# Optimization experiments

Hardware: AMD Instinct MI355X
Metric: run time of the kernel (lower is better)

## Reference

```python
import math
import jax, jax.numpy as jnp
import numpy as np
from jax import lax

B, M, L, DM = 4, 4, 1024, 768
DS, DCONV, LR = 8, 3, 16
D2 = DM // 2                # d_inner // 2 (expand=1)
DTR = math.ceil(DM / 16)    # dt_rank = 48
LN_EPS = 1e-5
RMS_EPS = 1e-5


def setup_inputs() -> dict:
    key = jax.random.key(0)
    ks = jax.random.split(key, 10)
    hidden_states = jax.random.normal(ks[0], (B, M, L, DM), jnp.float32)
    modality_index = jnp.arange(M, dtype=jnp.int32)
    in_w1 = jax.random.normal(ks[1], (M, LR, DM), jnp.float32) / np.sqrt(DM)
    in_ln_g = jnp.ones((M, LR), jnp.float32)
    in_ln_b = jnp.zeros((M, LR), jnp.float32)
    in_w2 = jax.random.normal(ks[2], (M, DM, LR), jnp.float32) / np.sqrt(LR)
    x_proj_w = jax.random.normal(ks[3], (DTR + 2 * DS, D2), jnp.float32) / np.sqrt(D2)
    dt_proj_w = jax.random.uniform(ks[4], (D2, DTR), jnp.float32, -DTR ** -0.5, DTR ** -0.5)
    dt = jnp.exp(jax.random.uniform(ks[5], (D2,), jnp.float32) * (np.log(0.1) - np.log(0.001)) + np.log(0.001))
    dt = jnp.clip(dt, 1e-4, None)
    dt_proj_b = dt + jnp.log(-jnp.expm1(-dt))   # inverse-softplus init
    A_log = jnp.log(jnp.broadcast_to(jnp.arange(1, DS + 1, dtype=jnp.float32), (D2, DS)))
    D = jnp.ones((D2,), jnp.float32)
    conv_x_w = jax.random.uniform(ks[6], (D2, 1, DCONV), jnp.float32, -DCONV ** -0.5, DCONV ** -0.5)
    conv_z_w = jax.random.uniform(ks[7], (D2, 1, DCONV), jnp.float32, -DCONV ** -0.5, DCONV ** -0.5)
    norm_w = jnp.ones((D2,), jnp.float32)
    out_w = jax.random.normal(ks[8], (M, DM, D2), jnp.float32) / np.sqrt(D2)
    scale = jnp.float32(1e-4)
    return dict(hidden_states=hidden_states, in_w1=in_w1, in_ln_g=in_ln_g, in_ln_b=in_ln_b,
                in_w2=in_w2, x_proj_w=x_proj_w, dt_proj_w=dt_proj_w, dt_proj_b=dt_proj_b,
                A_log=A_log, D=D, conv_x_w=conv_x_w, conv_z_w=conv_z_w, norm_w=norm_w,
                out_w=out_w, scale=scale, modality_index=modality_index)


def _dwconv_silu(x, w):
    # x: (b, d, L), w: (d, 1, k); depthwise 'same' conv (no bias: conv_bias//2 == 0) + SiLU
    y = lax.conv_general_dilated(x, w, (1,), 'SAME', feature_group_count=x.shape[1],
                                 dimension_numbers=('NCH', 'OIH', 'NCH'))
    return jax.nn.silu(y)


def _combine(e1, e2):
    a1, b1 = e1
    a2, b2 = e2
    return a1 * a2, a2 * b1 + b2


def reference(hidden_states, in_w1, in_ln_g, in_ln_b, in_w2, x_proj_w, dt_proj_w, dt_proj_b,
              A_log, D, conv_x_w, conv_z_w, norm_w, out_w, scale, modality_index):
    b, m, l, dm = hidden_states.shape
    d2 = conv_x_w.shape[0]
    dtr, ds = dt_proj_w.shape[1], A_log.shape[1]
    # --- per-modality low-rank in-projection: Linear -> LayerNorm -> GELU -> Linear ---
    w1 = jnp.take(in_w1, modality_index, axis=0)
    g = jnp.take(in_ln_g, modality_index, axis=0)[None, :, None, :]
    bta = jnp.take(in_ln_b, modality_index, axis=0)[None, :, None, :]
    w2 = jnp.take(in_w2, modality_index, axis=0)
    t = jnp.einsum('bmld,mrd->bmlr', hidden_states, w1)
    mu = t.mean(-1, keepdims=True)
    var = jnp.mean((t - mu) ** 2, -1, keepdims=True)
    t = (t - mu) * lax.rsqrt(var + LN_EPS) * g + bta
    t = jax.nn.gelu(t, approximate=False)
    xz = jnp.einsum('bmlr,mdr->bmld', t, w2)          # (b, m, l, d_inner)
    xz = xz.transpose(0, 2, 1, 3).reshape(b, l * m, -1)  # modality-interleaved, (b, Lm, d_inner)
    x, z = jnp.split(xz, 2, axis=-1)
    # --- depthwise conv + SiLU on both branches ---
    x = _dwconv_silu(x.transpose(0, 2, 1), conv_x_w)  # (b, d2, Lm)
    z = _dwconv_silu(z.transpose(0, 2, 1), conv_z_w)
    xT = x.transpose(0, 2, 1)  # (b, Lm, d2)
    zT = z.transpose(0, 2, 1)
    # --- input-dependent SSM parameters ---
    x_dbl = xT @ x_proj_w.T                              # (b, Lm, dtr+2*ds)
    dt, Bc, Cc = jnp.split(x_dbl, [dtr, dtr + ds], axis=-1)
    dt = dt @ dt_proj_w.T + dt_proj_b                    # Linear WITH bias (as in source)
    delta = jax.nn.softplus(dt + dt_proj_b)             # delta_bias added again (faithful)
    A = -jnp.exp(A_log)                                  # (d2, ds)
    dA = jnp.exp(delta[..., None] * A)                   # (b, Lm, d2, ds)
    dBx = delta[..., None] * Bc[:, :, None, :] * xT[..., None]
    # --- selective scan: h_t = dA_t * h_{t-1} + dBx_t ---
    _, h = lax.associative_scan(_combine, (dA, dBx), axis=1)
    y = jnp.einsum('blds,bls->bld', h, Cc) + D * xT      # (b, Lm, d2)
    # --- gated RMSNorm (norm before gate) ---
    y = y * lax.rsqrt(jnp.mean(y * y, -1, keepdims=True) + RMS_EPS) * norm_w
    y = y * jax.nn.silu(zT)
    # --- per-modality out-projection ---
    y = y.reshape(b, l, m, d2).transpose(0, 2, 1, 3)     # (b, m, l, d2)
    out = jnp.einsum('bmld,mod->bmlo', y, jnp.take(out_w, modality_index, axis=0))
    return out * scale
```

## Files before the change

### kernel.cpp

```cpp
#include <hip/hip_runtime.h>
#include <hip/hip_bf16.h>

#define LM   4096
#define D2   384
#define NCHK 64
#define TCHK 64

typedef __attribute__((ext_vector_type(8))) short short8b;
typedef __attribute__((ext_vector_type(4))) float f32x4;

__device__ __forceinline__ float siluf_(float x) { return x / (1.f + expf(-x)); }
__device__ __forceinline__ float softplusf_(float x) {
  return fmaxf(x, 0.f) + log1pf(expf(-fabsf(x)));
}
__device__ __forceinline__ short f2b_(float f) {
  __hip_bfloat16 h = __float2bfloat16(f);
  return *reinterpret_cast<short*>(&h);
}

__global__ __launch_bounds__(256) void k1a_proj(
    const float* __restrict__ hs, const float* __restrict__ w1g,
    const float* __restrict__ lng, const float* __restrict__ lnb,
    const int* __restrict__ midx, float* __restrict__ tbuf)
{
  __shared__ float w1s[16][772];
  const int tid = threadIdx.x;
  const int l0 = blockIdx.x * 16;
  const int m  = blockIdx.y;
  const int b  = blockIdx.z;
  const int mi = midx[m];
  {
    const float4* wp = (const float4*)(w1g + (size_t)mi * 16 * 768);
    for (int i = tid; i < 16 * 192; i += 256) {
      int r = i / 192, c = (i % 192) * 4;
      *(float4*)&w1s[r][c] = wp[i];
    }
  }
  __syncthreads();
  const int p = tid >> 4, r = tid & 15;
  const float* hrow = hs + (((size_t)(b * 4 + m)) * 1024 + l0 + p) * 768;
  float a0 = 0.f, a1 = 0.f, a2 = 0.f, a3 = 0.f;
  #pragma unroll 4
  for (int k = 0; k < 192; k += 4) {
    float4 x0 = *(const float4*)&hrow[(k + 0) * 4];
    float4 x1 = *(const float4*)&hrow[(k + 1) * 4];
    float4 x2 = *(const float4*)&hrow[(k + 2) * 4];
    float4 x3 = *(const float4*)&hrow[(k + 3) * 4];
    float4 w0 = *(const float4*)&w1s[r][(k + 0) * 4];
    float4 w1 = *(const float4*)&w1s[r][(k + 1) * 4];
    float4 w2 = *(const float4*)&w1s[r][(k + 2) * 4];
    float4 w3 = *(const float4*)&w1s[r][(k + 3) * 4];
    a0 += x0.x*w0.x + x0.y*w0.y + x0.z*w0.z + x0.w*w0.w;
    a1 += x1.x*w1.x + x1.y*w1.y + x1.z*w1.z + x1.w*w1.w;
    a2 += x2.x*w2.x + x2.y*w2.y + x2.z*w2.z + x2.w*w2.w;
    a3 += x3.x*w3.x + x3.y*w3.y + x3.z*w3.z + x3.w*w3.w;
  }
  const float acc = (a0 + a1) + (a2 + a3);
  float s = acc, q = acc * acc;
  #pragma unroll
  for (int msk = 1; msk < 16; msk <<= 1) {
    s += __shfl_xor(s, msk);
    q += __shfl_xor(q, msk);
  }
  const float mu  = s * (1.f / 16.f);
  const float var = q * (1.f / 16.f) - mu * mu;
  float v = (acc - mu) * rsqrtf(var + 1e-5f) * lng[mi * 16 + r] + lnb[mi * 16 + r];
  v = 0.5f * v * (1.f + erff(v * 0.70710678118654752f));
  tbuf[(((size_t)(b * 4 + m)) * 1024 + l0 + p) * 16 + r] = v;
}

__global__ __launch_bounds__(256) void k1b_xz(
    const float* __restrict__ tbuf, const float* __restrict__ w2g,
    const int* __restrict__ midx,
    float* __restrict__ xr, float* __restrict__ zr)
{
  __shared__ float ts[32][16];
  const int tid = threadIdx.x;
  const int l0 = blockIdx.x * 32;
  const int m  = blockIdx.y;
  const int b  = blockIdx.z;
  const int mi = midx[m];
  if (tid < 128) {
    float4 v = *(const float4*)&tbuf[(((size_t)(b * 4 + m)) * 1024 + l0) * 16 + tid * 4];
    *(float4*)&ts[tid >> 2][(tid & 3) * 4] = v;
  }
  float w2c[3][16];
  #pragma unroll
  for (int dd = 0; dd < 3; dd++) {
    const int d = tid + 256 * dd;
    #pragma unroll
    for (int rq = 0; rq < 4; rq++)
      *(float4*)&w2c[dd][rq * 4] = *(const float4*)&w2g[((size_t)mi * 768 + d) * 16 + rq * 4];
  }
  __syncthreads();
  for (int p = 0; p < 32; p++) {
    float tv[16];
    #pragma unroll
    for (int rq = 0; rq < 4; rq++) *(float4*)&tv[rq * 4] = *(const float4*)&ts[p][rq * 4];
    const int t = (l0 + p) * 4 + m;
    const size_t o = ((size_t)b * LM + t) * D2;
    #pragma unroll
    for (int dd = 0; dd < 3; dd++) {
      float a = 0.f;
      #pragma unroll
      for (int r2 = 0; r2 < 16; r2++) a += tv[r2] * w2c[dd][r2];
      const int d = tid + 256 * dd;
      if (d < D2) xr[o + d] = a;
      else        zr[o + d - D2] = a;
    }
  }
}

__global__ __launch_bounds__(256) void k2_xdbl(
    const float* __restrict__ xr, const float* __restrict__ xw,
    const float* __restrict__ cwx, float* __restrict__ xdbl)
{
  __shared__ float xcl[16][388];
  __shared__ float xws[32][388];
  const int tid = threadIdx.x;
  const int t0 = blockIdx.x * 16;
  const int b  = blockIdx.y;

  for (int i = tid; i < 16 * 384; i += 256) {
    const int tt = i / 384, d = i % 384;
    const int t = t0 + tt;
    const size_t base = (size_t)b * LM * D2 + d;
    float xm = (t > 0)      ? xr[base + (size_t)(t - 1) * D2] : 0.f;
    float x0 =                xr[base + (size_t)t * D2];
    float xp = (t + 1 < LM) ? xr[base + (size_t)(t + 1) * D2] : 0.f;
    float v = cwx[d * 3] * xm + cwx[d * 3 + 1] * x0 + cwx[d * 3 + 2] * xp;
    xcl[tt][d] = siluf_(v);
  }

  #pragma unroll
  for (int pass = 0; pass < 2; pass++) {
    if (pass) __syncthreads();
    {
      const float4* wp = (const float4*)(xw + (size_t)pass * 32 * 384);
      for (int i = tid; i < 32 * 96; i += 256) {
        int o = i / 96, c = (i % 96) * 4;
        *(float4*)&xws[o][c] = wp[i];
      }
    }
    __syncthreads();
    const int ks  = tid & 3;
    const int mt  = tid >> 2;
    const int og4 = mt & 7;
    const int ttg = mt >> 3;
    float acc[2][4] = {};
    for (int q = ks * 24; q < ks * 24 + 24; q++) {
      float4 a[2], w[4];
      #pragma unroll
      for (int i = 0; i < 2; i++) a[i] = *(const float4*)&xcl[ttg * 2 + i][q * 4];
      #pragma unroll
      for (int j = 0; j < 4; j++) w[j] = *(const float4*)&xws[og4 * 4 + j][q * 4];
      #pragma unroll
      for (int i = 0; i < 2; i++)
        #pragma unroll
        for (int j = 0; j < 4; j++)
          acc[i][j] += a[i].x * w[j].x + a[i].y * w[j].y + a[i].z * w[j].z + a[i].w * w[j].w;
    }
    #pragma unroll
    for (int i = 0; i < 2; i++)
      #pragma unroll
      for (int j = 0; j < 4; j++) {
        float v = acc[i][j];
        v += __shfl_xor(v, 1);  v += __shfl_xor(v, 2);
        acc[i][j] = v;
      }
    if (ks == 0) {
      #pragma unroll
      for (int i = 0; i < 2; i++) {
        float4 v4 = make_float4(acc[i][0], acc[i][1], acc[i][2], acc[i][3]);
        *(float4*)&xdbl[((size_t)b * LM + t0 + ttg * 2 + i) * 64 + pass * 32 + og4 * 4] = v4;
      }
    }
  }
}

__global__ __launch_bounds__(384) void k3_delta(
    const float* __restrict__ xdbl, const float* __restrict__ dtw,
    const float* __restrict__ dtb, float* __restrict__ delta)
{
  __shared__ float xt[32][48];
  const int tid = threadIdx.x;
  const int t0 = blockIdx.x * 32;
  const int b  = blockIdx.y;
  for (int i = tid; i < 32 * 12; i += 384) {
    int tt = i / 12, c = (i % 12) * 4;
    *(float4*)&xt[tt][c] = *(const float4*)&xdbl[((size_t)b * LM + t0 + tt) * 64 + c];
  }
  float wc[48];
  #pragma unroll
  for (int rq = 0; rq < 12; rq++)
    *(float4*)&wc[rq * 4] = *(const float4*)&dtw[(size_t)tid * 48 + rq * 4];
  const float bias2 = 2.f * dtb[tid];
  __syncthreads();
  for (int p = 0; p < 32; p++) {
    float acc = 0.f;
    #pragma unroll
    for (int r2 = 0; r2 < 48; r2++) acc += xt[p][r2] * wc[r2];
    delta[((size_t)b * LM + t0 + p) * D2 + tid] = softplusf_(acc + bias2);
  }
}

__global__ __launch_bounds__(768) void s1_scan(
    const float* __restrict__ xr, const float* __restrict__ delta,
    const float* __restrict__ xdbl, const float* __restrict__ alog,
    const float* __restrict__ cwx, float* __restrict__ aP, float* __restrict__ bAg)
{
  __shared__ float Bs[TCHK][8];
  const int tid = threadIdx.x;
  const int half = tid >= 384 ? 1 : 0;
  const int d = tid - half * 384;
  const int c = blockIdx.x, b = blockIdx.y;
  const int t0 = c * TCHK;
  for (int i = tid; i < TCHK * 8; i += 768) {
    const int tt = i >> 3, s = i & 7;
    Bs[tt][s] = xdbl[((size_t)b * LM + t0 + tt) * 64 + 48 + s];
  }
  float a[4];
  #pragma unroll
  for (int s = 0; s < 4; s++) a[s] = -expf(alog[d * 8 + half * 4 + s]);
  const float w0 = cwx[d * 3], w1 = cwx[d * 3 + 1], w2 = cwx[d * 3 + 2];
  const float* xp = xr + (size_t)b * LM * D2 + d;
  const float* dp = delta + (size_t)b * LM * D2 + d;
  float xm = (t0 > 0) ? xp[(size_t)(t0 - 1) * D2] : 0.f;
  float x0 = xp[(size_t)t0 * D2];
  float h[4] = {};
  float ap[4] = {1.f, 1.f, 1.f, 1.f};
  __syncthreads();
  for (int tt = 0; tt < TCHK; tt++) {
    const int t = t0 + tt;
    const float xn = (t + 1 < LM) ? xp[(size_t)(t + 1) * D2] : 0.f;
    const float xc = siluf_(w0 * xm + w1 * x0 + w2 * xn);
    const float dv = dp[(size_t)t * D2];
    #pragma unroll
    for (int s = 0; s < 4; s++) {
      const float dA = expf(dv * a[s]);
      ap[s] *= dA;
      h[s] = dA * h[s] + (dv * Bs[tt][half * 4 + s]) * xc;
    }
    xm = x0; x0 = xn;
  }
  const size_t o = (((size_t)b * NCHK + c) * 8 + half * 4) * D2 + d;
  #pragma unroll
  for (int s = 0; s < 4; s++) { aP[o + (size_t)s * D2] = ap[s]; bAg[o + (size_t)s * D2] = h[s]; }
}

__global__ __launch_bounds__(256) void s2_combine(
    const float* __restrict__ aP, const float* __restrict__ bAg, float* __restrict__ hI)
{
  const int idx = blockIdx.x * 256 + threadIdx.x;
  const int d = idx % 384;
  const int s = (idx / 384) & 7;
  const int b = idx / 3072;
  float h = 0.f;
  for (int c = 0; c < NCHK; c++) {
    const size_t o = (((size_t)b * NCHK + c) * 8 + s) * D2 + d;
    const float av = aP[o], bv = bAg[o];
    hI[o] = h;
    h = av * h + bv;
  }
}

__global__ __launch_bounds__(256) void wconv(
    const float* __restrict__ w, short* __restrict__ w16)
{
  const int i = (blockIdx.x * 256 + threadIdx.x) * 4;
  const float4 v = *(const float4*)&w[i];
  ushort4 o;
  o.x = (unsigned short)f2b_(v.x);
  o.y = (unsigned short)f2b_(v.y);
  o.z = (unsigned short)f2b_(v.z);
  o.w = (unsigned short)f2b_(v.w);
  *(ushort4*)&w16[i] = o;
}

__global__ __launch_bounds__(384) void s3_rescan(
    const float* __restrict__ xr, const float* __restrict__ zr,
    const float* delta_in, const float* __restrict__ xdbl,
    const float* __restrict__ hI, const float* __restrict__ alog,
    const float* __restrict__ cwx, const float* __restrict__ cwz,
    const float* __restrict__ Dv, const float* __restrict__ nw,
    float* Yg)
{
  __shared__ float Bs[TCHK][8];
  __shared__ float Cs[TCHK][8];
  __shared__ float yt[32][389];
  __shared__ float part[32][12];
  __shared__ float rinv[32];
  const int tid = threadIdx.x;
  const int d = tid;
  const int c = blockIdx.x, b = blockIdx.y;
  const int t0 = c * TCHK;
  for (int i = tid; i < TCHK * 8; i += 384) {
    const int tt = i >> 3, s = i & 7;
    const size_t o = ((size_t)b * LM + t0 + tt) * 64;
    Bs[tt][s] = xdbl[o + 48 + s];
    Cs[tt][s] = xdbl[o + 56 + s];
  }
  float a[8];
  #pragma unroll
  for (int s = 0; s < 8; s++) a[s] = -expf(alog[d * 8 + s]);
  float h[8];
  const size_t ho = (((size_t)b * NCHK + c) * 8) * D2 + d;
  #pragma unroll
  for (int s = 0; s < 8; s++) h[s] = hI[ho + (size_t)s * D2];
  const float wx0 = cwx[d * 3], wx1 = cwx[d * 3 + 1], wx2 = cwx[d * 3 + 2];
  const float wz0 = cwz[d * 3], wz1 = cwz[d * 3 + 1], wz2 = cwz[d * 3 + 2];
  const float Dd = Dv[d], nwd = nw[d];
  const float* xp = xr + (size_t)b * LM * D2 + d;
  const float* zp = zr + (size_t)b * LM * D2 + d;
  const float* dp = delta_in + (size_t)b * LM * D2 + d;
  float xm = (t0 > 0) ? xp[(size_t)(t0 - 1) * D2] : 0.f;
  float x0 = xp[(size_t)t0 * D2];
  float zm = (t0 > 0) ? zp[(size_t)(t0 - 1) * D2] : 0.f;
  float z0 = zp[(size_t)t0 * D2];
  __syncthreads();

  #pragma unroll
  for (int H = 0; H < 2; H++) {
    const int tb = t0 + H * 32;
    for (int tt = 0; tt < 32; tt++) {
      const int t = tb + tt;
      const float xn = (t + 1 < LM) ? xp[(size_t)(t + 1) * D2] : 0.f;
      const float xc = siluf_(wx0 * xm + wx1 * x0 + wx2 * xn);
      const float dv = dp[(size_t)t * D2];
      float yv = 0.f;
      #pragma unroll
      for (int s = 0; s < 8; s++) {
        const float dA = expf(dv * a[s]);
        h[s] = dA * h[s] + (dv * Bs[H * 32 + tt][s]) * xc;
        yv += h[s] * Cs[H * 32 + tt][s];
      }
      yv += Dd * xc;
      yt[tt][d] = yv;
      xm = x0; x0 = xn;
    }
    __syncthreads();
    {
      const int tr = tid & 31, j = tid >> 5;
      float sum = 0.f;
      #pragma unroll
      for (int k = 0; k < 32; k++) { const float v = yt[tr][j * 32 + k]; sum += v * v; }
      part[tr][j] = sum;
    }
    __syncthreads();
    if (tid < 32) {
      float sm = 0.f;
      #pragma unroll
      for (int j = 0; j < 12; j++) sm += part[tid][j];
      rinv[tid] = rsqrtf(sm * (1.f / 384.f) + 1e-5f);
    }
    __syncthreads();
    for (int tt = 0; tt < 32; tt++) {
      const int t = tb + tt;
      const float zn = (t + 1 < LM) ? zp[(size_t)(t + 1) * D2] : 0.f;
      const float zc = siluf_(siluf_(wz0 * zm + wz1 * z0 + wz2 * zn));
      Yg[((size_t)b * LM + t) * D2 + d] = yt[tt][d] * rinv[tt] * nwd * zc;
      zm = z0; z0 = zn;
    }
    __syncthreads();
  }
}

__global__ __launch_bounds__(256) void k4_mfma(
    const float* __restrict__ Yg, const short* __restrict__ W16,
    const int* __restrict__ midx, const float* __restrict__ scalep,
    float* __restrict__ out)
{
  const int tid = threadIdx.x;
  const int wid = tid >> 6, lane = tid & 63;
  const int lt = blockIdx.x, ot = blockIdx.y, bm = blockIdx.z;
  const int b = bm >> 2, m = bm & 3;
  const int mi = midx[m];
  const int l0 = lt * 128, o0 = ot * 128;
  const int wr = wid >> 1, wc = wid & 1;
  const int lr = lane & 15, lg = lane >> 4;
  const float scale = scalep[0];

  const float* Ab = Yg + (size_t)b * LM * D2;
  const short* Bb = W16 + (size_t)mi * 768 * D2;

  f32x4 acc[4][4];
  #pragma unroll
  for (int i = 0; i < 4; i++)
    #pragma unroll
    for (int j = 0; j < 4; j++) acc[i][j] = (f32x4){0.f, 0.f, 0.f, 0.f};

  for (int k0 = 0; k0 < D2; k0 += 32) {
    const int kk = k0 + lg * 8;
    short8b afr[4], bfr[4];
    #pragma unroll
    for (int mr = 0; mr < 4; mr++) {
      const int row = l0 + wr * 64 + mr * 16 + lr;
      const float* ap = Ab + (size_t)(row * 4 + m) * D2 + kk;
      const f32x4 a0 = *(const f32x4*)ap;
      const f32x4 a1 = *(const f32x4*)(ap + 4);
      short8b af;
      af[0] = f2b_(a0.x); af[1] = f2b_(a0.y); af[2] = f2b_(a0.z); af[3] = f2b_(a0.w);
      af[4] = f2b_(a1.x); af[5] = f2b_(a1.y); af[6] = f2b_(a1.z); af[7] = f2b_(a1.w);
      afr[mr] = af;
    }
    #pragma unroll
    for (int nr = 0; nr < 4; nr++) {
      const int col = o0 + wc * 64 + nr * 16 + lr;
      bfr[nr] = *(const short8b*)(Bb + (size_t)col * D2 + kk);
    }
    #pragma unroll
    for (int mr = 0; mr < 4; mr++)
      #pragma unroll
      for (int nr = 0; nr < 4; nr++)
        acc[mr][nr] = __builtin_amdgcn_mfma_f32_16x16x32_bf16(
            afr[mr], bfr[nr], acc[mr][nr], 0, 0, 0);
  }

  #pragma unroll
  for (int mr = 0; mr < 4; mr++) {
    #pragma unroll
    for (int r = 0; r < 4; r++) {
      const int row = l0 + wr * 64 + mr * 16 + lg * 4 + r;
      const size_t ob = (((size_t)(b * 4 + m)) * 1024 + row) * 768;
      #pragma unroll
      for (int nr = 0; nr < 4; nr++) {
        const int col = o0 + wc * 64 + nr * 16 + lr;
        out[ob + col] = acc[mr][nr][r] * scale;
      }
    }
  }
}

extern "C" void kernel_launch(void* const* d_in, const int* in_sizes, int n_in,
                              void* d_out, int out_size, void* d_ws, size_t ws_size,
                              hipStream_t stream)
{
  const float* hs   = (const float*)d_in[0];
  const float* w1   = (const float*)d_in[1];
  const float* lng  = (const float*)d_in[2];
  const float* lnb  = (const float*)d_in[3];
  const float* w2   = (const float*)d_in[4];
  const float* xw   = (const float*)d_in[5];
  const float* dtw  = (const float*)d_in[6];
  const float* dtb  = (const float*)d_in[7];
  const float* alog = (const float*)d_in[8];
  const float* Dv   = (const float*)d_in[9];
  const float* cwx  = (const float*)d_in[10];
  const float* cwz  = (const float*)d_in[11];
  const float* nw   = (const float*)d_in[12];
  const float* ow   = (const float*)d_in[13];
  const float* sc   = (const float*)d_in[14];
  const int*   midx = (const int*)d_in[15];
  float* out = (float*)d_out;

  float* ws = (float*)d_ws;
  const size_t NE = (size_t)4 * LM * D2;
  float* xr    = ws;
  float* zr    = xr + NE;
  float* delta = zr + NE;
  float* xdbl  = delta + NE;
  float* aP    = xdbl + (size_t)4 * LM * 64;
  float* bAg   = aP + (size_t)4 * NCHK * 8 * D2;
  float* hI    = bAg + (size_t)4 * NCHK * 8 * D2;
  float* tbuf  = aP;
  short* owb16 = (short*)aP;

  k1a_proj<<<dim3(64, 4, 4), 256, 0, stream>>>(hs, w1, lng, lnb, midx, tbuf);
  k1b_xz<<<dim3(32, 4, 4), 256, 0, stream>>>(tbuf, w2, midx, xr, zr);
  k2_xdbl<<<dim3(256, 4), 256, 0, stream>>>(xr, xw, cwx, xdbl);
  k3_delta<<<dim3(128, 4), 384, 0, stream>>>(xdbl, dtw, dtb, delta);
  s1_scan<<<dim3(NCHK, 4), 768, 0, stream>>>(xr, delta, xdbl, alog, cwx, aP, bAg);
  s2_combine<<<48, 256, 0, stream>>>(aP, bAg, hI);
  wconv<<<1152, 256, 0, stream>>>(ow, owb16);
  s3_rescan<<<dim3(NCHK, 4), 384, 0, stream>>>(xr, zr, delta, xdbl, hI, alog, cwx, cwz, Dv, nw, delta);
  k4_mfma<<<dim3(8, 6, 16), 256, 0, stream>>>(delta, owb16, midx, sc, out);
}
```

Before: 462.6 us.

## Halve scan chunk size, derive dA by powers of one exp, reuse output buffer

Scan chunks drop from 64 to 32 timesteps, doubling the blocks in s1_scan and s3_rescan, so the serial per-thread chain is shorter and more work is in flight. When A rows are geometric (A_s = (s+1)·A_1, detected at runtime), the per-state exps are replaced by one exp plus repeated multiplications, with a fallback to per-state exp otherwise. The chunk carries now live in the output buffer and s2 writes the prefix in place, freeing workspace. In exchange the s2 serial combine chain doubles in length, and the power products may differ slightly in rounding from separate exps.

```diff
diff --git a/kernel.cpp b/kernel.cpp
--- a/kernel.cpp
+++ b/kernel.cpp
@@ -1,10 +1,10 @@
 #include <hip/hip_runtime.h>
 #include <hip/hip_bf16.h>
 
-#define LM   4096
-#define D2   384
-#define NCHK 64
-#define TCHK 64
+#define LM    4096
+#define D2    384
+#define NCHK2 128
+#define TC2   32
 
 typedef __attribute__((ext_vector_type(8))) short short8b;
 typedef __attribute__((ext_vector_type(4))) float f32x4;
@@ -209,19 +209,25 @@
     const float* __restrict__ xdbl, const float* __restrict__ alog,
     const float* __restrict__ cwx, float* __restrict__ aP, float* __restrict__ bAg)
 {
-  __shared__ float Bs[TCHK][8];
+  __shared__ float Bs[TC2][8];
   const int tid = threadIdx.x;
   const int half = tid >= 384 ? 1 : 0;
   const int d = tid - half * 384;
   const int c = blockIdx.x, b = blockIdx.y;
-  const int t0 = c * TCHK;
-  for (int i = tid; i < TCHK * 8; i += 768) {
-    const int tt = i >> 3, s = i & 7;
+  const int t0 = c * TC2;
+  if (tid < TC2 * 8) {
+    const int tt = tid >> 3, s = tid & 7;
     Bs[tt][s] = xdbl[((size_t)b * LM + t0 + tt) * 64 + 48 + s];
   }
+  const float a1 = -expf(alog[d * 8]);
   float a[4];
-  #pragma unroll
-  for (int s = 0; s < 4; s++) a[s] = -expf(alog[d * 8 + half * 4 + s]);
+  bool geo = true;
+  #pragma unroll
+  for (int s = 0; s < 4; s++) {
+    a[s] = -expf(alog[d * 8 + half * 4 + s]);
+    const float ex = (float)(half * 4 + s + 1) * a1;
+    geo = geo && (fabsf(a[s] - ex) <= 1e-4f * fabsf(a[s]));
+  }
   const float w0 = cwx[d * 3], w1 = cwx[d * 3 + 1], w2 = cwx[d * 3 + 2];
   const float* xp = xr + (size_t)b * LM * D2 + d;
   const float* dp = delta + (size_t)b * LM * D2 + d;
@@ -230,36 +236,48 @@
   float h[4] = {};
   float ap[4] = {1.f, 1.f, 1.f, 1.f};
   __syncthreads();
-  for (int tt = 0; tt < TCHK; tt++) {
+  #pragma unroll 4
+  for (int tt = 0; tt < TC2; tt++) {
     const int t = t0 + tt;
     const float xn = (t + 1 < LM) ? xp[(size_t)(t + 1) * D2] : 0.f;
     const float xc = siluf_(w0 * xm + w1 * x0 + w2 * xn);
     const float dv = dp[(size_t)t * D2];
+    float dA[4];
+    if (geo) {
+      const float q = expf(dv * a1);
+      const float q2 = q * q, q4 = q2 * q2;
+      if (half == 0) { dA[0] = q;      dA[1] = q2;      dA[2] = q2 * q;      dA[3] = q4; }
+      else           { dA[0] = q4 * q; dA[1] = q4 * q2; dA[2] = q4 * q2 * q; dA[3] = q4 * q4; }
+    } else {
+      #pragma unroll
+      for (int s = 0; s < 4; s++) dA[s] = expf(dv * a[s]);
+    }
+    const float dx = dv * xc;
     #pragma unroll
     for (int s = 0; s < 4; s++) {
-      const float dA = expf(dv * a[s]);
-      ap[s] *= dA;
-      h[s] = dA * h[s] + (dv * Bs[tt][half * 4 + s]) * xc;
+      ap[s] *= dA[s];
+      h[s] = dA[s] * h[s] + dx * Bs[tt][half * 4 + s];
     }
     xm = x0; x0 = xn;
   }
-  const size_t o = (((size_t)b * NCHK + c) * 8 + half * 4) * D2 + d;
+  const size_t o = (((size_t)b * NCHK2 + c) * 8 + half * 4) * D2 + d;
   #pragma unroll
   for (int s = 0; s < 4; s++) { aP[o + (size_t)s * D2] = ap[s]; bAg[o + (size_t)s * D2] = h[s]; }
 }
 
 __global__ __launch_bounds__(256) void s2_combine(
-    const float* __restrict__ aP, const float* __restrict__ bAg, float* __restrict__ hI)
+    float* __restrict__ aP, const float* __restrict__ bAg)
 {
   const int idx = blockIdx.x * 256 + threadIdx.x;
   const int d = idx % 384;
   const int s = (idx / 384) & 7;
   const int b = idx / 3072;
   float h = 0.f;
-  for (int c = 0; c < NCHK; c++) {
-    const size_t o = (((size_t)b * NCHK + c) * 8 + s) * D2 + d;
+  #pragma unroll 4
+  for (int c = 0; c < NCHK2; c++) {
+    const size_t o = (((size_t)b * NCHK2 + c) * 8 + s) * D2 + d;
     const float av = aP[o], bv = bAg[o];
-    hI[o] = h;
+    aP[o] = h;
     h = av * h + bv;
   }
 }
@@ -285,26 +303,32 @@
     const float* __restrict__ Dv, const float* __restrict__ nw,
     float* Yg)
 {
-  __shared__ float Bs[TCHK][8];
-  __shared__ float Cs[TCHK][8];
-  __shared__ float yt[32][389];
-  __shared__ float part[32][12];
-  __shared__ float rinv[32];
+  __shared__ float Bs[TC2][8];
+  __shared__ float Cs[TC2][8];
+  __shared__ float yt[TC2][389];
+  __shared__ float part[TC2][12];
+  __shared__ float rinv[TC2];
   const int tid = threadIdx.x;
   const int d = tid;
   const int c = blockIdx.x, b = blockIdx.y;
-  const int t0 = c * TCHK;
-  for (int i = tid; i < TCHK * 8; i += 384) {
-    const int tt = i >> 3, s = i & 7;
+  const int t0 = c * TC2;
+  if (tid < TC2 * 8) {
+    const int tt = tid >> 3, s = tid & 7;
     const size_t o = ((size_t)b * LM + t0 + tt) * 64;
     Bs[tt][s] = xdbl[o + 48 + s];
     Cs[tt][s] = xdbl[o + 56 + s];
   }
+  const float a1 = -expf(alog[d * 8]);
   float a[8];
-  #pragma unroll
-  for (int s = 0; s < 8; s++) a[s] = -expf(alog[d * 8 + s]);
+  bool geo = true;
+  #pragma unroll
+  for (int s = 0; s < 8; s++) {
+    a[s] = -expf(alog[d * 8 + s]);
+    const float ex = (float)(s + 1) * a1;
+    geo = geo && (fabsf(a[s] - ex) <= 1e-4f * fabsf(a[s]));
+  }
   float h[8];
-  const size_t ho = (((size_t)b * NCHK + c) * 8) * D2 + d;
+  const size_t ho = (((size_t)b * NCHK2 + c) * 8) * D2 + d;
   #pragma unroll
   for (int s = 0; s < 8; s++) h[s] = hI[ho + (size_t)s * D2];
   const float wx0 = cwx[d * 3], wx1 = cwx[d * 3 + 1], wx2 = cwx[d * 3 + 2];
@@ -315,53 +339,60 @@
   const float* dp = delta_in + (size_t)b * LM * D2 + d;
   float xm = (t0 > 0) ? xp[(size_t)(t0 - 1) * D2] : 0.f;
   float x0 = xp[(size_t)t0 * D2];
+  __syncthreads();
+
+  #pragma unroll 4
+  for (int tt = 0; tt < TC2; tt++) {
+    const int t = t0 + tt;
+    const float xn = (t + 1 < LM) ? xp[(size_t)(t + 1) * D2] : 0.f;
+    const float xc = siluf_(wx0 * xm + wx1 * x0 + wx2 * xn);
+    const float dv = dp[(size_t)t * D2];
+    float dA[8];
+    if (geo) {
+      const float q = expf(dv * a1);
+      const float q2 = q * q, q4 = q2 * q2;
+      dA[0] = q;      dA[1] = q2;      dA[2] = q2 * q;      dA[3] = q4;
+      dA[4] = q4 * q; dA[5] = q4 * q2; dA[6] = q4 * q2 * q; dA[7] = q4 * q4;
+    } else {
+      #pragma unroll
+      for (int s = 0; s < 8; s++) dA[s] = expf(dv * a[s]);
+    }
+    const float dx = dv * xc;
+    float yv = 0.f;
+    #pragma unroll
+    for (int s = 0; s < 8; s++) {
+      h[s] = dA[s] * h[s] + dx * Bs[tt][s];
+      yv += h[s] * Cs[tt][s];
+    }
+    yv += Dd * xc;
+    yt[tt][d] = yv;
+    xm = x0; x0 = xn;
+  }
+  __syncthreads();
+  {
+    const int tr = tid & 31, j = tid >> 5;
+    float sum = 0.f;
+    #pragma unroll
+    for (int k = 0; k < 32; k++) { const float v = yt[tr][j * 32 + k]; sum += v * v; }
+    part[tr][j] = sum;
+  }
+  __syncthreads();
+  if (tid < TC2) {
+    float sm = 0.f;
+    #pragma unroll
+    for (int j = 0; j < 12; j++) sm += part[tid][j];
+    rinv[tid] = rsqrtf(sm * (1.f / 384.f) + 1e-5f);
+  }
+  __syncthreads();
   float zm = (t0 > 0) ? zp[(size_t)(t0 - 1) * D2] : 0.f;
   float z0 = zp[(size_t)t0 * D2];
-  __syncthreads();
-
-  #pragma unroll
-  for (int H = 0; H < 2; H++) {
-    const int tb = t0 + H * 32;
-    for (int tt = 0; tt < 32; tt++) {
-      const int t = tb + tt;
-      const float xn = (t + 1 < LM) ? xp[(size_t)(t + 1) * D2] : 0.f;
-      const float xc = siluf_(wx0 * xm + wx1 * x0 + wx2 * xn);
-      const float dv = dp[(size_t)t * D2];
-      float yv = 0.f;
-      #pragma unroll
-      for (int s = 0; s < 8; s++) {
-        const float dA = expf(dv * a[s]);
-        h[s] = dA * h[s] + (dv * Bs[H * 32 + tt][s]) * xc;
-        yv += h[s] * Cs[H * 32 + tt][s];
-      }
-      yv += Dd * xc;
-      yt[tt][d] = yv;
-      xm = x0; x0 = xn;
-    }
-    __syncthreads();
-    {
-      const int tr = tid & 31, j = tid >> 5;
-      float sum = 0.f;
-      #pragma unroll
-      for (int k = 0; k < 32; k++) { const float v = yt[tr][j * 32 + k]; sum += v * v; }
-      part[tr][j] = sum;
-    }
-    __syncthreads();
-    if (tid < 32) {
-      float sm = 0.f;
-      #pragma unroll
-      for (int j = 0; j < 12; j++) sm += part[tid][j];
-      rinv[tid] = rsqrtf(sm * (1.f / 384.f) + 1e-5f);
-    }
-    __syncthreads();
-    for (int tt = 0; tt < 32; tt++) {
-      const int t = tb + tt;
-      const float zn = (t + 1 < LM) ? zp[(size_t)(t + 1) * D2] : 0.f;
-      const float zc = siluf_(siluf_(wz0 * zm + wz1 * z0 + wz2 * zn));
-      Yg[((size_t)b * LM + t) * D2 + d] = yt[tt][d] * rinv[tt] * nwd * zc;
-      zm = z0; z0 = zn;
-    }
-    __syncthreads();
+  #pragma unroll 4
+  for (int tt = 0; tt < TC2; tt++) {
+    const int t = t0 + tt;
+    const float zn = (t + 1 < LM) ? zp[(size_t)(t + 1) * D2] : 0.f;
+    const float zc = siluf_(siluf_(wz0 * zm + wz1 * z0 + wz2 * zn));
+    Yg[((size_t)b * LM + t) * D2 + d] = yt[tt][d] * rinv[tt] * nwd * zc;
+    zm = z0; z0 = zn;
   }
 }
 
@@ -459,19 +490,20 @@
   float* zr    = xr + NE;
   float* delta = zr + NE;
   float* xdbl  = delta + NE;
-  float* aP    = xdbl + (size_t)4 * LM * 64;
-  float* bAg   = aP + (size_t)4 * NCHK * 8 * D2;
-  float* hI    = bAg + (size_t)4 * NCHK * 8 * D2;
-  float* tbuf  = aP;
-  short* owb16 = (short*)aP;
+  float* tbuf  = xdbl + (size_t)4 * LM * 64;
+  short* owb16 = (short*)tbuf;
+
+  float* aP  = out;
+  float* bAg = aP + (size_t)4 * NCHK2 * 8 * D2;
+  float* hI  = aP;
 
   k1a_proj<<<dim3(64, 4, 4), 256, 0, stream>>>(hs, w1, lng, lnb, midx, tbuf);
   k1b_xz<<<dim3(32, 4, 4), 256, 0, stream>>>(tbuf, w2, midx, xr, zr);
   k2_xdbl<<<dim3(256, 4), 256, 0, stream>>>(xr, xw, cwx, xdbl);
   k3_delta<<<dim3(128, 4), 384, 0, stream>>>(xdbl, dtw, dtb, delta);
-  s1_scan<<<dim3(NCHK, 4), 768, 0, stream>>>(xr, delta, xdbl, alog, cwx, aP, bAg);
-  s2_combine<<<48, 256, 0, stream>>>(aP, bAg, hI);
+  s1_scan<<<dim3(NCHK2, 4), 768, 0, stream>>>(xr, delta, xdbl, alog, cwx, aP, bAg);
+  s2_combine<<<48, 256, 0, stream>>>(aP, bAg);
   wconv<<<1152, 256, 0, stream>>>(ow, owb16);
-  s3_rescan<<<dim3(NCHK, 4), 384, 0, stream>>>(xr, zr, delta, xdbl, hI, alog, cwx, cwz, Dv, nw, delta);
+  s3_rescan<<<dim3(NCHK2, 4), 384, 0, stream>>>(xr, zr, delta, xdbl, hI, alog, cwx, cwz, Dv, nw, delta);
   k4_mfma<<<dim3(8, 6, 16), 256, 0, stream>>>(delta, owb16, midx, sc, out);
 }
```

Result: faster. 425.2 us (-8.1%).
